# Optimization experiments

Hardware: AMD Instinct MI355X
Metric: run time of the kernel (lower is better)

The kernel has to match this reference:

```python
import jax, jax.numpy as jnp
import numpy as np

IMAGE_SIZE = 256
NEAR = 0.1
FAR = 100.0
EPS = 1e-3
BACKGROUND = jnp.array([0.0, 0.0, 0.0], dtype=jnp.float32)
CHUNK = 64  # faces processed per scan step (keeps [B,CHUNK,3,P] intermediate ~100MB)


def setup_inputs() -> dict:
    key = jax.random.key(0)
    k1, k2, k3, k4 = jax.random.split(key, 4)
    B, F, T = 2, 4096, 4
    # small triangles in NDC with z in (near, far)
    centers = jax.random.uniform(k1, (B, F, 1, 2), minval=-1.0, maxval=1.0)
    offsets = 0.15 * jax.random.normal(k2, (B, F, 3, 2))
    xy = centers + offsets
    z = jax.random.uniform(k3, (B, F, 1, 1), minval=1.0, maxval=20.0) \
        + 0.1 * jax.random.normal(k4, (B, F, 3, 1))
    faces = jnp.concatenate([xy, z], axis=-1).astype(jnp.float32)  # [B,F,3,3]
    textures = jax.random.uniform(jax.random.fold_in(key, 7), (B, F, T, T, T, 3),
                                  dtype=jnp.float32)
    return {"faces": faces, "textures": textures}


def _pixel_grid(is_):
    c = (2.0 * jnp.arange(is_, dtype=jnp.float32) + 1.0 - is_) / is_
    # kernel iterates rows top->bottom with y flipped (y up in NDC)
    yp, xp = jnp.meshgrid(-c, c, indexing="ij")  # [H,W]
    return xp.reshape(-1), yp.reshape(-1)  # [P]


def _raster_chunk(fchunk, xp, yp, near, far):
    # fchunk: [B,C,3verts,3coords]; xp,yp: [P]
    x = fchunk[..., 0]
    y = fchunk[..., 1]
    z = fchunk[..., 2]  # [B,C,3]
    x0, x1, x2 = x[..., 0:1], x[..., 1:2], x[..., 2:3]
    y0, y1, y2 = y[..., 0:1], y[..., 1:2], y[..., 2:3]

    # inside test: pixel on the CCW side of all 3 edges (back faces culled)
    def edge(ya, xa, yb, xb):
        return (yp - ya) * (xb - xa) - (xp - xa) * (yb - ya)  # [B,C,P]
    inside = (edge(y0, x0, y1, x1) >= 0) & (edge(y1, x1, y2, x2) >= 0) \
             & (edge(y2, x2, y0, x0) >= 0)

    # inverse of [[x0,y0,1],[x1,y1,1],[x2,y2,1]] via adjugate (as in CUDA kernel)
    x0s, x1s, x2s = x[..., 0], x[..., 1], x[..., 2]
    y0s, y1s, y2s = y[..., 0], y[..., 1], y[..., 2]
    det = x2s * (y0s - y1s) + x0s * (y1s - y2s) + x1s * (y2s - y0s)
    det = jnp.where(det >= 0, jnp.maximum(det, 1e-10), jnp.minimum(det, -1e-10))
    inv = jnp.stack([
        jnp.stack([y1s - y2s, x2s - x1s, x1s * y2s - x2s * y1s], -1),
        jnp.stack([y2s - y0s, x0s - x2s, x2s * y0s - x0s * y2s], -1),
        jnp.stack([y0s - y1s, x1s - x0s, x0s * y1s - x1s * y0s], -1),
    ], -2) / det[..., None, None]  # [B,C,3,3]

    # barycentric weights per pixel: [B,C,3,P]
    w = inv[..., 0, None] * xp + inv[..., 1, None] * yp + inv[..., 2, None]
    w = jnp.clip(w, 0.0, 1.0)
    w = w / jnp.maximum(w.sum(axis=2, keepdims=True), 1e-10)

    # perspective-correct depth: 1/zp = sum_k w_k / z_k
    inv_zp = (w / z[..., None]).sum(axis=2)  # [B,C,P]
    zp = 1.0 / jnp.maximum(inv_zp, 1e-10)
    valid = inside & (zp > near) & (zp < far)
    zp = jnp.where(valid, zp, far)
    return zp, jnp.moveaxis(w, 2, 3)  # zp:[B,C,P], w:[B,C,P,3]


def _rasterize_maps(faces, image_size, near, far):
    B, F = faces.shape[:2]
    P = image_size * image_size
    xp, yp = _pixel_grid(image_size)
    n_chunks = F // CHUNK
    fch = faces.reshape(B, n_chunks, CHUNK, 3, 3).transpose(1, 0, 2, 3, 4)
    ids = jnp.arange(F, dtype=jnp.int32).reshape(n_chunks, CHUNK)
    init = (jnp.full((B, P), far, jnp.float32),        # best depth (z-buffer)
            jnp.full((B, P), -1, jnp.int32),            # best face index
            jnp.zeros((B, P, 3), jnp.float32))          # best barycentric weights

    def step(carry, inp):
        bz, bf, bw = carry
        fchunk, idc = inp
        zp, w = _raster_chunk(fchunk, xp, yp, near, far)
        am = jnp.argmin(zp, axis=1)  # [B,P] nearest face within chunk
        zmin = jnp.take_along_axis(zp, am[:, None, :], axis=1)[:, 0]          # [B,P]
        wsel = jnp.take_along_axis(w, am[:, None, :, None], axis=1)[:, 0]     # [B,P,3]
        fsel = idc[am]                                                        # [B,P]
        upd = zmin < bz
        return (jnp.where(upd, zmin, bz),
                jnp.where(upd, fsel, bf),
                jnp.where(upd[..., None], wsel, bw)), None

    (bz, bf, bw), _ = jax.lax.scan(jax.checkpoint(step), init, (fch, ids))
    return bf, bw, bz  # face_index_map, weight_map, depth_map (flat pixels)


def _forward(faces, textures):
    B, F = faces.shape[:2]
    T = textures.shape[2]
    is_ = IMAGE_SIZE
    P = is_ * is_
    fidx, w, zp = _rasterize_maps(faces, is_, NEAR, FAR)
    mask = fidx >= 0
    fi = jnp.maximum(fidx, 0)

    # per-pixel vertex depths of hit face: [B,P,3]
    faces_z = faces[..., 2]
    fz = jax.vmap(lambda a, i: a[i])(faces_z, fi)

    # texture cube coords with perspective correction (as in CUDA kernel)
    tif = jnp.clip(w * (T - 1) * (zp[..., None] / fz), 0.0, T - 1 - EPS)
    lo = jnp.floor(tif).astype(jnp.int32)
    frac = tif - lo

    tex_flat = textures.reshape(B, F, T * T * T, 3)
    rgb = jnp.zeros((B, P, 3), jnp.float32)
    for pn in range(8):  # trilinear blend over 8 cube corners
        bits = [(pn >> k) & 1 for k in range(3)]
        idx = lo + jnp.array(bits, jnp.int32)
        wc = jnp.ones_like(frac[..., 0])
        for k in range(3):
            wc = wc * (frac[..., k] if bits[k] else (1.0 - frac[..., k]))
        lin = (idx[..., 0] * T + idx[..., 1]) * T + idx[..., 2]
        texel = jax.vmap(lambda tf, f, l: tf[f, l])(tex_flat, fi, lin)  # [B,P,3]
        rgb = rgb + wc[..., None] * texel

    rgb = jnp.where(mask[..., None], rgb, BACKGROUND)
    alpha = mask.astype(jnp.float32)
    return (rgb.reshape(B, is_, is_, 3),
            alpha.reshape(B, is_, is_),
            zp.reshape(B, is_, is_))


def reference(faces, textures):
    return _forward(faces, textures)
```

## Files before the change

kernel.cpp:

```cpp
#include <hip/hip_runtime.h>

#define IS 256
#define FNUM 4096
#define BATCH 2
#define NSPLIT 16
#define FSPLIT (FNUM / NSPLIT)
#define FAR_ 100.0f
#define NEAR_ 0.1f


__global__ __launch_bounds__(256, 8) void raster_kernel(
    const float* __restrict__ faces, int* __restrict__ keys)
{
#pragma clang fp contract(off)
  __shared__ float rec[256 * 12];
  __shared__ int cnt[4];

  const int tid = threadIdx.x;
  const int wid = tid >> 6, lane = tid & 63;
  const int z = blockIdx.z;
  const int b = z >> 4;
  const int split = z & 15;

  const int qx = tid & 15, qy = tid >> 4;
  const int col0 = blockIdx.x * 32 + qx * 2;
  const int row0 = blockIdx.y * 32 + qy * 2;

  const float xpA = (2.0f * (float)col0 + 1.0f - 256.0f) * (1.0f / 256.0f);
  const float xpB = (2.0f * (float)(col0 + 1) + 1.0f - 256.0f) * (1.0f / 256.0f);
  const float ypA = -((2.0f * (float)row0 + 1.0f - 256.0f) * (1.0f / 256.0f));
  const float ypB = -((2.0f * (float)(row0 + 1) + 1.0f - 256.0f) * (1.0f / 256.0f));

  const float txmin = (2.0f * (float)(blockIdx.x * 32) + 1.0f - 256.0f) * (1.0f / 256.0f) - 1e-3f;
  const float txmax = (2.0f * (float)(blockIdx.x * 32 + 31) + 1.0f - 256.0f) * (1.0f / 256.0f) + 1e-3f;
  const float tymax = -((2.0f * (float)(blockIdx.y * 32) + 1.0f - 256.0f) * (1.0f / 256.0f)) + 1e-3f;
  const float tymin = -((2.0f * (float)(blockIdx.y * 32 + 31) + 1.0f - 256.0f) * (1.0f / 256.0f)) - 1e-3f;

  const int f = split * FSPLIT + tid;
  const float* fp = faces + ((size_t)b * FNUM + f) * 9;
  const float x0 = fp[0], y0 = fp[1], z0 = fp[2];
  const float x1 = fp[3], y1 = fp[4], z1 = fp[5];
  const float x2 = fp[6], y2 = fp[7], z2 = fp[8];

  const float det = x2 * (y0 - y1) + x0 * (y1 - y2) + x1 * (y2 - y0);
  const float minx = fminf(fminf(x0, x1), x2), maxx = fmaxf(fmaxf(x0, x1), x2);
  const float miny = fminf(fminf(y0, y1), y2), maxy = fmaxf(fmaxf(y0, y1), y2);
  const bool keep = (det >= -1e-5f) &&
                    (minx <= txmax) && (maxx >= txmin) &&
                    (miny <= tymax) && (maxy >= tymin);

  const unsigned long long m = __ballot(keep);
  if (lane == 0) cnt[wid] = __popcll(m);
  __syncthreads();
  const int total = cnt[0] + cnt[1] + cnt[2] + cnt[3];
  if (keep) {
    int base = 0;
    for (int w = 0; w < wid; ++w) base += cnt[w];
    const int pos = base + __popcll(m & ((1ull << lane) - 1ull));
    const float cd = (det >= 0.0f) ? fmaxf(det, 1e-10f) : fminf(det, -1e-10f);
    const float rdet = __builtin_amdgcn_rcpf(cd);
    const float u0 = __builtin_amdgcn_rcpf(z0) * rdet;
    const float u1 = __builtin_amdgcn_rcpf(z1) * rdet;
    const float u2 = __builtin_amdgcn_rcpf(z2) * rdet;
    float4* r4 = (float4*)&rec[pos * 12];
    r4[0] = make_float4(x0, y0, x1, y1);
    r4[1] = make_float4(x2, y2, u0, u1);
    r4[2] = make_float4(u2, __int_as_float(f ^ 0xFFF), 0.0f, 0.0f);
  }
  __syncthreads();

  int kAA = 0, kAB = 0, kBA = 0, kBB = 0;
  for (int i = 0; i < total; ++i) {
    const float4 r0 = ((const float4*)rec)[i * 3 + 0];
    const float4 r1 = ((const float4*)rec)[i * 3 + 1];
    const float4 r2 = ((const float4*)rec)[i * 3 + 2];
    const float fx0 = r0.x, fy0 = r0.y, fx1 = r0.z, fy1 = r0.w;
    const float fx2 = r1.x, fy2 = r1.y, u0 = r1.z, u1 = r1.w;
    const float u2 = r2.x;
    const int fidx = __float_as_int(r2.y);

    const float t01x = fx1 - fx0, t01y = fy1 - fy0;
    const float t12x = fx2 - fx1, t12y = fy2 - fy1;
    const float t20x = fx0 - fx2, t20y = fy0 - fy2;

    const float a01A = (ypA - fy0) * t01x, a01B = (ypB - fy0) * t01x;
    const float b01A = (xpA - fx0) * t01y, b01B = (xpB - fx0) * t01y;
    const float a12A = (ypA - fy1) * t12x, a12B = (ypB - fy1) * t12x;
    const float b12A = (xpA - fx1) * t12y, b12B = (xpB - fx1) * t12y;
    const float a20A = (ypA - fy2) * t20x, a20B = (ypB - fy2) * t20x;
    const float b20A = (xpA - fx2) * t20y, b20B = (xpB - fx2) * t20y;

#define PX(KK, AR, AC)                                                        \
    {                                                                         \
      const float e01 = a01##AR - b01##AC;                                    \
      const float e12 = a12##AR - b12##AC;                                    \
      const float e20 = a20##AR - b20##AC;                                    \
      const bool inside = fminf(fminf(e01, e12), e20) >= 0.0f;                \
      const float izp = fmaf(e12, u0, fmaf(e20, u1, e01 * u2));               \
      const bool valid = inside && (izp > 0.01f) && (izp < 10.0f);            \
      const int key =                                                         \
          valid ? (int)((__float_as_uint(izp) & 0xFFFFF000u)) | fidx : 0;     \
      KK = (key > KK) ? key : KK;                                             \
    }
    PX(kAA, A, A) PX(kAB, A, B) PX(kBA, B, A) PX(kBB, B, B)
#undef PX
  }

  const int pbase = b * 65536 + row0 * 256 + col0;
  if (kAA) atomicMax(&keys[pbase], kAA);
  if (kAB) atomicMax(&keys[pbase + 1], kAB);
  if (kBA) atomicMax(&keys[pbase + 256], kBA);
  if (kBB) atomicMax(&keys[pbase + 257], kBB);
}

__global__ __launch_bounds__(256) void resolve_kernel(
    const float* __restrict__ faces, const float* __restrict__ tex,
    float* __restrict__ out_rgb, float* __restrict__ out_alpha,
    float* __restrict__ out_z)
{
#pragma clang fp contract(off)
  const int p = blockIdx.x * 256 + threadIdx.x;
  const int b = p >> 16;
  const int pi = p & 65535;
  const int row = pi >> 8, col = pi & 255;

  const int key = ((const int*)out_alpha)[p];
  if (key < 0x30000000) {
    out_rgb[(size_t)p * 3 + 0] = 0.0f;
    out_rgb[(size_t)p * 3 + 1] = 0.0f;
    out_rgb[(size_t)p * 3 + 2] = 0.0f;
    out_alpha[p] = 0.0f;
    out_z[p] = FAR_;
    return;
  }

  const int fid = (key & 0xFFF) ^ 0xFFF;
  const float xp = (2.0f * (float)col + 1.0f - 256.0f) * (1.0f / 256.0f);
  const float yp = -((2.0f * (float)row + 1.0f - 256.0f) * (1.0f / 256.0f));

  const float* fp = faces + ((size_t)b * FNUM + fid) * 9;
  const float x0 = fp[0], y0 = fp[1], z0 = fp[2];
  const float x1 = fp[3], y1 = fp[4], z1 = fp[5];
  const float x2 = fp[6], y2 = fp[7], z2 = fp[8];

  const float det = x2 * (y0 - y1) + x0 * (y1 - y2) + x1 * (y2 - y0);
  const float cd = (det >= 0.0f) ? fmaxf(det, 1e-10f) : fminf(det, -1e-10f);
  const float rdet = __builtin_amdgcn_rcpf(cd);
  const float rz0 = __builtin_amdgcn_rcpf(z0);
  const float rz1 = __builtin_amdgcn_rcpf(z1);
  const float rz2 = __builtin_amdgcn_rcpf(z2);

  const float e01 = (yp - y0) * (x1 - x0) - (xp - x0) * (y1 - y0);
  const float e12 = (yp - y1) * (x2 - x1) - (xp - x1) * (y2 - y1);
  const float e20 = (yp - y2) * (x0 - x2) - (xp - x2) * (y0 - y2);

  const float c0 = fminf(fmaxf(e12 * rdet, 0.0f), 1.0f);
  const float c1 = fminf(fmaxf(e20 * rdet, 0.0f), 1.0f);
  const float c2 = fminf(fmaxf(e01 * rdet, 0.0f), 1.0f);
  const float s = fmaxf((c0 + c1) + c2, 1e-10f);
  const float rs = __builtin_amdgcn_rcpf(s);
  const float w0 = c0 * rs, w1 = c1 * rs, w2 = c2 * rs;
  const float izp = (w0 * rz0 + w1 * rz1) + w2 * rz2;
  const float zp = __builtin_amdgcn_rcpf(fmaxf(izp, 1e-10f));

  const float t0 = fminf(fmaxf((w0 * 3.0f) * (zp * rz0), 0.0f), 2.999f);
  const float t1 = fminf(fmaxf((w1 * 3.0f) * (zp * rz1), 0.0f), 2.999f);
  const float t2 = fminf(fmaxf((w2 * 3.0f) * (zp * rz2), 0.0f), 2.999f);
  const float l0 = floorf(t0), l1 = floorf(t1), l2 = floorf(t2);
  const int i0 = (int)l0, i1 = (int)l1, i2 = (int)l2;
  const float fr0 = t0 - l0, fr1 = t1 - l1, fr2 = t2 - l2;
  const float g0 = 1.0f - fr0, g1 = 1.0f - fr1, g2 = 1.0f - fr2;

  const float* tb = tex + ((size_t)b * FNUM + fid) * 192;
  float rr = 0.f, rg = 0.f, rb = 0.f;
#pragma unroll
  for (int pn = 0; pn < 4; ++pn) {
    const int b0 = pn & 1, b1 = (pn >> 1) & 1;
    const float w01 = (b0 ? fr0 : g0) * (b1 ? fr1 : g1);
    const float wz0 = w01 * g2, wz1 = w01 * fr2;
    const int lin0 = ((i0 + b0) * 4 + (i1 + b1)) * 4 + i2;
    const float* tp = tb + lin0 * 3;
    rr = rr + wz0 * tp[0] + wz1 * tp[3];
    rg = rg + wz0 * tp[1] + wz1 * tp[4];
    rb = rb + wz0 * tp[2] + wz1 * tp[5];
  }

  out_rgb[(size_t)p * 3 + 0] = rr;
  out_rgb[(size_t)p * 3 + 1] = rg;
  out_rgb[(size_t)p * 3 + 2] = rb;
  out_alpha[p] = 1.0f;
  out_z[p] = zp;
}

extern "C" void kernel_launch(void* const* d_in, const int* in_sizes, int n_in,
                              void* d_out, int out_size, void* d_ws, size_t ws_size,
                              hipStream_t stream) {
  const float* faces = (const float*)d_in[0];
  const float* tex   = (const float*)d_in[1];
  float* out = (float*)d_out;
  float* out_rgb   = out;
  float* out_alpha = out + 393216;
  float* out_z     = out + 393216 + 131072;

  dim3 gridA(IS / 32, IS / 32, BATCH * NSPLIT);
  hipLaunchKernelGGL(raster_kernel, gridA, dim3(256), 0, stream,
                     faces, (int*)out_alpha);

  dim3 gridC((BATCH * IS * IS) / 256, 1, 1);
  hipLaunchKernelGGL(resolve_kernel, gridC, dim3(256), 0, stream,
                     faces, tex, out_rgb, out_alpha, out_z);
}
```

Measured before the change: 72.74 us.

## Bin faces per 16x16 wavefront sub-tile to skip non-overlapping faces

Remaps each wavefront to its own 16x16 sub-tile of the 32x32 block and builds per-sub-tile face lists in shared memory with atomic counters. Each wavefront then iterates only over faces whose bounding box overlaps its sub-tile, not all faces kept for the block. This trades shared-memory atomics and one extra indirect LDS load per face for fewer edge tests per wavefront. Since the list order comes from atomics, correctness relies on the depth/index key comparison being order-independent.

Result: faster. 70.26 us (median of 2 runs) (-3.4%).

```diff
diff --git a/kernel.cpp b/kernel.cpp
--- a/kernel.cpp
+++ b/kernel.cpp
@@ -14,7 +14,9 @@
 {
 #pragma clang fp contract(off)
   __shared__ float rec[256 * 12];
+  __shared__ int slist[4 * 256];
   __shared__ int cnt[4];
+  __shared__ int scnt[4];
 
   const int tid = threadIdx.x;
   const int wid = tid >> 6, lane = tid & 63;
@@ -22,19 +24,25 @@
   const int b = z >> 4;
   const int split = z & 15;
 
-  const int qx = tid & 15, qy = tid >> 4;
-  const int col0 = blockIdx.x * 32 + qx * 2;
-  const int row0 = blockIdx.y * 32 + qy * 2;
+  const int sx = wid & 1, sy = wid >> 1;
+  const int qx = lane & 7, qy = lane >> 3;
+  const int col0 = blockIdx.x * 32 + sx * 16 + qx * 2;
+  const int row0 = blockIdx.y * 32 + sy * 16 + qy * 2;
 
   const float xpA = (2.0f * (float)col0 + 1.0f - 256.0f) * (1.0f / 256.0f);
   const float xpB = (2.0f * (float)(col0 + 1) + 1.0f - 256.0f) * (1.0f / 256.0f);
   const float ypA = -((2.0f * (float)row0 + 1.0f - 256.0f) * (1.0f / 256.0f));
   const float ypB = -((2.0f * (float)(row0 + 1) + 1.0f - 256.0f) * (1.0f / 256.0f));
 
-  const float txmin = (2.0f * (float)(blockIdx.x * 32) + 1.0f - 256.0f) * (1.0f / 256.0f) - 1e-3f;
-  const float txmax = (2.0f * (float)(blockIdx.x * 32 + 31) + 1.0f - 256.0f) * (1.0f / 256.0f) + 1e-3f;
-  const float tymax = -((2.0f * (float)(blockIdx.y * 32) + 1.0f - 256.0f) * (1.0f / 256.0f)) + 1e-3f;
-  const float tymin = -((2.0f * (float)(blockIdx.y * 32 + 31) + 1.0f - 256.0f) * (1.0f / 256.0f)) - 1e-3f;
+  const int bx32 = blockIdx.x * 32, by32 = blockIdx.y * 32;
+  const float sx0min = (2.0f * (float)(bx32) + 1.0f - 256.0f) * (1.0f / 256.0f) - 1e-3f;
+  const float sx0max = (2.0f * (float)(bx32 + 15) + 1.0f - 256.0f) * (1.0f / 256.0f) + 1e-3f;
+  const float sx1min = (2.0f * (float)(bx32 + 16) + 1.0f - 256.0f) * (1.0f / 256.0f) - 1e-3f;
+  const float sx1max = (2.0f * (float)(bx32 + 31) + 1.0f - 256.0f) * (1.0f / 256.0f) + 1e-3f;
+  const float sy0max = -((2.0f * (float)(by32) + 1.0f - 256.0f) * (1.0f / 256.0f)) + 1e-3f;
+  const float sy0min = -((2.0f * (float)(by32 + 15) + 1.0f - 256.0f) * (1.0f / 256.0f)) - 1e-3f;
+  const float sy1max = -((2.0f * (float)(by32 + 16) + 1.0f - 256.0f) * (1.0f / 256.0f)) + 1e-3f;
+  const float sy1min = -((2.0f * (float)(by32 + 31) + 1.0f - 256.0f) * (1.0f / 256.0f)) - 1e-3f;
 
   const int f = split * FSPLIT + tid;
   const float* fp = faces + ((size_t)b * FNUM + f) * 9;
@@ -45,14 +53,17 @@
   const float det = x2 * (y0 - y1) + x0 * (y1 - y2) + x1 * (y2 - y0);
   const float minx = fminf(fminf(x0, x1), x2), maxx = fmaxf(fmaxf(x0, x1), x2);
   const float miny = fminf(fminf(y0, y1), y2), maxy = fmaxf(fmaxf(y0, y1), y2);
-  const bool keep = (det >= -1e-5f) &&
-                    (minx <= txmax) && (maxx >= txmin) &&
-                    (miny <= tymax) && (maxy >= tymin);
+
+  const bool ox0 = (minx <= sx0max) && (maxx >= sx0min);
+  const bool ox1 = (minx <= sx1max) && (maxx >= sx1min);
+  const bool oy0 = (miny <= sy0max) && (maxy >= sy0min);
+  const bool oy1 = (miny <= sy1max) && (maxy >= sy1min);
+  const bool keep = (det >= -1e-5f) && (ox0 || ox1) && (oy0 || oy1);
 
   const unsigned long long m = __ballot(keep);
   if (lane == 0) cnt[wid] = __popcll(m);
+  if (tid < 4) scnt[tid] = 0;
   __syncthreads();
-  const int total = cnt[0] + cnt[1] + cnt[2] + cnt[3];
   if (keep) {
     int base = 0;
     for (int w = 0; w < wid; ++w) base += cnt[w];
@@ -66,14 +77,21 @@
     r4[0] = make_float4(x0, y0, x1, y1);
     r4[1] = make_float4(x2, y2, u0, u1);
     r4[2] = make_float4(u2, __int_as_float(f ^ 0xFFF), 0.0f, 0.0f);
+    if (ox0 && oy0) slist[0 * 256 + atomicAdd(&scnt[0], 1)] = pos;
+    if (ox1 && oy0) slist[1 * 256 + atomicAdd(&scnt[1], 1)] = pos;
+    if (ox0 && oy1) slist[2 * 256 + atomicAdd(&scnt[2], 1)] = pos;
+    if (ox1 && oy1) slist[3 * 256 + atomicAdd(&scnt[3], 1)] = pos;
   }
   __syncthreads();
 
+  const int n = scnt[wid];
+  const int* mylist = &slist[wid * 256];
   int kAA = 0, kAB = 0, kBA = 0, kBB = 0;
-  for (int i = 0; i < total; ++i) {
-    const float4 r0 = ((const float4*)rec)[i * 3 + 0];
-    const float4 r1 = ((const float4*)rec)[i * 3 + 1];
-    const float4 r2 = ((const float4*)rec)[i * 3 + 2];
+  for (int i = 0; i < n; ++i) {
+    const int idx = mylist[i];
+    const float4 r0 = ((const float4*)rec)[idx * 3 + 0];
+    const float4 r1 = ((const float4*)rec)[idx * 3 + 1];
+    const float4 r2 = ((const float4*)rec)[idx * 3 + 2];
     const float fx0 = r0.x, fy0 = r0.y, fx1 = r0.z, fy1 = r0.w;
     const float fx2 = r1.x, fy2 = r1.y, u0 = r1.z, u1 = r1.w;
     const float u2 = r2.x;
```
